# Optimization experiments

Hardware: AMD Instinct MI355X
Metric: run time of the kernel (lower is better)

The kernel has to match this reference:

```python
import jax, jax.numpy as jnp
import numpy as np

N_NODES = 100000
N_EDGES = 1600000
D_FEAT = 64
NUM_LAYERS = 3


def setup_inputs() -> dict:
    key = jax.random.key(0)
    k1, k2, k3, k4 = jax.random.split(key, 4)
    X = jax.random.normal(k1, (N_NODES, D_FEAT), dtype=jnp.float32)
    src = jax.random.randint(k2, (N_EDGES,), 0, N_NODES, dtype=jnp.int32)
    dst = jax.random.randint(k3, (N_EDGES,), 0, N_NODES, dtype=jnp.int32)
    ew = jax.random.uniform(k4, (N_EDGES,), dtype=jnp.float32)
    return {"X": X, "src": src, "dst": dst, "ew": ew}


def _spmm(X, src, dst, ew):
    # gather source features, scale by edge weight, scatter-sum into dst
    msgs = X[src] * ew[:, None]  # [E, d]
    return jax.ops.segment_sum(msgs, dst, num_segments=N_NODES)


def reference(X, src, dst, ew):
    # LightGCNConv with stack_layers=True: average of layer-0..num_layers embeddings
    X_list = [X]
    h = X
    for _ in range(NUM_LAYERS):
        h = _spmm(h, src, dst, ew)
        X_list.append(h)
    return jnp.mean(jnp.stack(X_list, axis=1), axis=1)  # [N, d]
```

## Files before the change

kernel.cpp:

```cpp
#include <hip/hip_runtime.h>
#include <hip/hip_fp16.h>

#define N_NODES 100000
#define D_FEAT  64
#define N_EDGES 1600000
#define NPB     128
#define NBUCK   ((N_NODES + NPB - 1) / NPB)
#define CAP     3072
#define CVT_BLOCKS  256
#define CVT_THREADS 1024
#define CHUNK   (N_EDGES / CVT_BLOCKS)
#define PULL_BLOCKS 2048
#define WCAP    64
#define SORT_CAP CAP

__global__ void init_bcur(int* __restrict__ bcur) {
    int t = threadIdx.x;
    if (t < NBUCK) bcur[t] = 0;
}

__global__ __launch_bounds__(CVT_THREADS) void cvt_part(const float* __restrict__ X,
                                                        __half* __restrict__ Xh,
                                                        const int* __restrict__ src,
                                                        const int* __restrict__ dst,
                                                        const float* __restrict__ ew,
                                                        int* __restrict__ bcur,
                                                        int2* __restrict__ bedges) {
    __shared__ int h[NBUCK];
    const int t = threadIdx.x;
    for (int i = t; i < NBUCK; i += CVT_THREADS) h[i] = 0;

    const int n4 = N_NODES * D_FEAT / 4;
    for (int i = blockIdx.x * CVT_THREADS + t; i < n4; i += CVT_BLOCKS * CVT_THREADS) {
        float4 v = ((const float4*)X)[i];
        ((__half2*)Xh)[2 * i]     = __floats2half2_rn(v.x, v.y);
        ((__half2*)Xh)[2 * i + 1] = __floats2half2_rn(v.z, v.w);
    }
    __syncthreads();

    const int beg = blockIdx.x * CHUNK, end = beg + CHUNK;
    for (int i = beg + t; i < end; i += CVT_THREADS)
        atomicAdd(&h[dst[i] >> 7], 1);
    __syncthreads();

    for (int i = t; i < NBUCK; i += CVT_THREADS) {
        int c = h[i];
        h[i] = c ? atomicAdd(&bcur[i], c) : 0;
    }
    __syncthreads();

    for (int i = beg + t; i < end; i += CVT_THREADS) {
        int d = dst[i];
        int b = d >> 7;
        int p = atomicAdd(&h[b], 1);
        if (p < CAP) {
            int2 e;
            e.x = src[i] | ((d & (NPB - 1)) << 17);
            e.y = __float_as_int(ew[i]);
            bedges[(size_t)b * CAP + p] = e;
        }
    }
}

__global__ void scan_bcnt(const int* __restrict__ bcnt, int* __restrict__ bptr,
                          int* __restrict__ row_ptr) {
    __shared__ int tmp[1024];
    const int t = threadIdx.x;
    int v = (t < NBUCK) ? bcnt[t] : 0;
    if (v > CAP) v = CAP;
    tmp[t] = v;
    __syncthreads();
    for (int off = 1; off < 1024; off <<= 1) {
        int u = (t >= off) ? tmp[t - off] : 0;
        __syncthreads();
        tmp[t] += u;
        __syncthreads();
    }
    if (t < NBUCK) bptr[t] = tmp[t] - v;
    if (t == NBUCK - 1) {
        bptr[NBUCK] = tmp[t];
        row_ptr[N_NODES] = tmp[t];
    }
}

__global__ __launch_bounds__(256) void sort_bucket(const int2* __restrict__ bedges,
                                                   const int* __restrict__ bcnt,
                                                   const int* __restrict__ bptr,
                                                   int2* __restrict__ sedges,
                                                   int* __restrict__ row_ptr) {
    __shared__ int cnt[NPB], sc[NPB], cur[NPB];
    __shared__ int2 buf[SORT_CAP];
    const int b = blockIdx.x, t = threadIdx.x;
    const int ibeg = b * CAP;
    const int obeg = bptr[b];
    int n = bcnt[b];
    if (n > CAP) n = CAP;

    if (t < NPB) cnt[t] = 0;
    __syncthreads();
    for (int i = t; i < n; i += 256) {
        int2 e = bedges[ibeg + i];
        buf[i] = e;
        atomicAdd(&cnt[e.x >> 17], 1);
    }
    __syncthreads();

    if (t < NPB) sc[t] = cnt[t];
    __syncthreads();
    for (int off = 1; off < NPB; off <<= 1) {
        int v = (t >= off && t < NPB) ? sc[t - off] : 0;
        __syncthreads();
        if (t < NPB) sc[t] += v;
        __syncthreads();
    }
    if (t < NPB) {
        cur[t] = sc[t] - cnt[t];
        int node = b * NPB + t;
        if (node < N_NODES) row_ptr[node] = obeg + sc[t] - cnt[t];
    }
    __syncthreads();

    for (int i = t; i < n; i += 256) {
        int2 e = buf[i];
        int p = atomicAdd(&cur[e.x >> 17], 1);
        sedges[obeg + p] = make_int2(e.x & 0x1FFFF, e.y);
    }
}

template <int MODE>
__global__ __launch_bounds__(256) void spmm_pull(const __half* __restrict__ hprev,
                                                 const int* __restrict__ row_ptr,
                                                 const int2* __restrict__ edges,
                                                 __half* __restrict__ hout,
                                                 float* __restrict__ out,
                                                 const float* __restrict__ X,
                                                 const __half* __restrict__ h1,
                                                 const __half* __restrict__ h2) {
    __shared__ int2 ebuf[4][WCAP];
    const int t    = threadIdx.x;
    const int wid  = t >> 6;
    const int lane = t & 63;
    const int half = lane >> 5;
    const int sub  = lane & 31;
    const int gw     = blockIdx.x * 4 + wid;
    const int nwaves = gridDim.x * 4;

    for (int node = gw; node < N_NODES; node += nwaves) {
        int2 bp = *(const int2*)&row_ptr[node];
        const int beg = bp.x, end = bp.y;
        const int d = end - beg;

        if (d <= WCAP) {
            const int dp = (d + 15) & ~15;
            if (lane < dp) {
                int2 e = (lane < d) ? edges[beg + lane] : make_int2(0, 0);
                ebuf[wid][lane] = e;
            }
            float ax = 0.0f, ay = 0.0f;
            const int nb = dp >> 4;
            for (int bi = 0; bi < nb; ++bi) {
                const int base = bi * 16 + half;
                unsigned tv[8]; float w[8];
                #pragma unroll
                for (int k = 0; k < 8; ++k) {
                    int2 e = ebuf[wid][base + 2 * k];
                    w[k]  = __int_as_float(e.y);
                    tv[k] = *(const unsigned*)(hprev + (((size_t)e.x << 6) | (2 * sub)));
                }
                #pragma unroll
                for (int k = 0; k < 8; ++k) {
                    float2 f = __half22float2(*(__half2*)&tv[k]);
                    ax += f.x * w[k];
                    ay += f.y * w[k];
                }
            }
            ax += __shfl_xor(ax, 32);
            ay += __shfl_xor(ay, 32);
            if (half == 0) {
                size_t bo = (size_t)node * 32 + sub;
                if (MODE == 2) {
                    float2 x  = ((const float2*)X)[bo];
                    float2 f1 = __half22float2(((const __half2*)h1)[bo]);
                    float2 f2 = __half22float2(((const __half2*)h2)[bo]);
                    ((float2*)out)[bo] = make_float2((x.x + f1.x + f2.x + ax) * 0.25f,
                                                     (x.y + f1.y + f2.y + ay) * 0.25f);
                } else {
                    ((__half2*)hout)[bo] = __floats2half2_rn(ax, ay);
                }
            }
        } else {
            float ax = 0.0f, ay = 0.0f;
            for (int j = beg; j < end; j += 16) {
                unsigned tv[8]; float w[8];
                #pragma unroll
                for (int k = 0; k < 8; ++k) {
                    int i0 = j + 2 * k, i1 = i0 + 1;
                    int2 e0 = edges[(i0 < end) ? i0 : beg];
                    int2 e1 = edges[(i1 < end) ? i1 : beg];
                    int s = half ? e1.x : e0.x;
                    float w0 = (i0 < end) ? __int_as_float(e0.y) : 0.0f;
                    float w1 = (i1 < end) ? __int_as_float(e1.y) : 0.0f;
                    w[k] = half ? w1 : w0;
                    tv[k] = *(const unsigned*)(hprev + (((size_t)s << 6) | (2 * sub)));
                }
                #pragma unroll
                for (int k = 0; k < 8; ++k) {
                    float2 f = __half22float2(*(__half2*)&tv[k]);
                    ax += f.x * w[k];
                    ay += f.y * w[k];
                }
            }
            ax += __shfl_xor(ax, 32);
            ay += __shfl_xor(ay, 32);
            if (half == 0) {
                size_t bo = (size_t)node * 32 + sub;
                if (MODE == 2) {
                    float2 x  = ((const float2*)X)[bo];
                    float2 f1 = __half22float2(((const __half2*)h1)[bo]);
                    float2 f2 = __half22float2(((const __half2*)h2)[bo]);
                    ((float2*)out)[bo] = make_float2((x.x + f1.x + f2.x + ax) * 0.25f,
                                                     (x.y + f1.y + f2.y + ay) * 0.25f);
                } else {
                    ((__half2*)hout)[bo] = __floats2half2_rn(ax, ay);
                }
            }
        }
    }
}

extern "C" void kernel_launch(void* const* d_in, const int* in_sizes, int n_in,
                              void* d_out, int out_size, void* d_ws, size_t ws_size,
                              hipStream_t stream) {
    const float* X   = (const float*)d_in[0];
    const int*   src = (const int*)  d_in[1];
    const int*   dst = (const int*)  d_in[2];
    const float* ew  = (const float*)d_in[3];
    float* out = (float*)d_out;

    const size_t feat = (size_t)N_NODES * D_FEAT;

    char* p = (char*)d_ws;
    __half* hA     = (__half*)p; p += feat * sizeof(__half);
    __half* hB     = (__half*)p; p += feat * sizeof(__half);
    __half* Xh     = (__half*)p; p += feat * sizeof(__half);
    int2*  sedges  = (int2*)p;   p += (size_t)N_EDGES * sizeof(int2);
    int*   row_ptr = (int*)p;    p += ((size_t)N_NODES + 1) * 4;
    int*   bcur    = (int*)p;    p += (size_t)NBUCK * 4;
    int*   bptr    = (int*)p;    p += ((size_t)NBUCK + 1) * 4;

    int2* bedges = (int2*)hA;

    init_bcur <<<1, 1024, 0, stream>>>(bcur);
    cvt_part  <<<CVT_BLOCKS, CVT_THREADS, 0, stream>>>(X, Xh, src, dst, ew, bcur, bedges);
    scan_bcnt <<<1, 1024, 0, stream>>>(bcur, bptr, row_ptr);
    sort_bucket<<<NBUCK, 256, 0, stream>>>(bedges, bcur, bptr, sedges, row_ptr);

    spmm_pull<0><<<PULL_BLOCKS, 256, 0, stream>>>(Xh, row_ptr, sedges, hA, out, X, hA, hB);
    spmm_pull<1><<<PULL_BLOCKS, 256, 0, stream>>>(hA, row_ptr, sedges, hB, out, X, hA, hB);
    spmm_pull<2><<<PULL_BLOCKS, 256, 0, stream>>>(hB, row_ptr, sedges, (__half*)nullptr, out, X, hA, hB);
}
```

Baseline: 229.6 us.

## Drop bucket scan kernel, sort buckets in place, use per-node (offset,count) pointers

Removes the single-block scan kernel by keeping edges in fixed-capacity per-bucket slots and sorting each bucket in place, with per-node (start, degree) pairs replacing the compacted row_ptr. The partition kernel now uses 500 blocks with each thread handling exactly four edges via vectorized int4 loads. This saves a kernel launch and a serial scan, and avoids a separate compacted edge buffer. In exchange the edge array is sparse (padded to CAP per bucket), which the SpMM loop reads only through the node pointers.

```diff
diff --git a/kernel.cpp b/kernel.cpp
--- a/kernel.cpp
+++ b/kernel.cpp
@@ -7,12 +7,11 @@
 #define NPB     128
 #define NBUCK   ((N_NODES + NPB - 1) / NPB)
 #define CAP     3072
-#define CVT_BLOCKS  256
+#define CVT_BLOCKS  500
 #define CVT_THREADS 1024
 #define CHUNK   (N_EDGES / CVT_BLOCKS)
 #define PULL_BLOCKS 2048
 #define WCAP    64
-#define SORT_CAP CAP
 
 __global__ void init_bcur(int* __restrict__ bcur) {
     int t = threadIdx.x;
@@ -25,7 +24,7 @@
                                                         const int* __restrict__ dst,
                                                         const float* __restrict__ ew,
                                                         int* __restrict__ bcur,
-                                                        int2* __restrict__ bedges) {
+                                                        int2* __restrict__ edges_p) {
     __shared__ int h[NBUCK];
     const int t = threadIdx.x;
     for (int i = t; i < NBUCK; i += CVT_THREADS) h[i] = 0;
@@ -38,68 +37,55 @@
     }
     __syncthreads();
 
-    const int beg = blockIdx.x * CHUNK, end = beg + CHUNK;
-    for (int i = beg + t; i < end; i += CVT_THREADS)
-        atomicAdd(&h[dst[i] >> 7], 1);
-    __syncthreads();
-
-    for (int i = t; i < NBUCK; i += CVT_THREADS) {
-        int c = h[i];
-        h[i] = c ? atomicAdd(&bcur[i], c) : 0;
-    }
-    __syncthreads();
-
-    for (int i = beg + t; i < end; i += CVT_THREADS) {
-        int d = dst[i];
-        int b = d >> 7;
-        int p = atomicAdd(&h[b], 1);
-        if (p < CAP) {
-            int2 e;
-            e.x = src[i] | ((d & (NPB - 1)) << 17);
-            e.y = __float_as_int(ew[i]);
-            bedges[(size_t)b * CAP + p] = e;
-        }
-    }
-}
-
-__global__ void scan_bcnt(const int* __restrict__ bcnt, int* __restrict__ bptr,
-                          int* __restrict__ row_ptr) {
-    __shared__ int tmp[1024];
-    const int t = threadIdx.x;
-    int v = (t < NBUCK) ? bcnt[t] : 0;
-    if (v > CAP) v = CAP;
-    tmp[t] = v;
-    __syncthreads();
-    for (int off = 1; off < 1024; off <<= 1) {
-        int u = (t >= off) ? tmp[t - off] : 0;
-        __syncthreads();
-        tmp[t] += u;
-        __syncthreads();
-    }
-    if (t < NBUCK) bptr[t] = tmp[t] - v;
-    if (t == NBUCK - 1) {
-        bptr[NBUCK] = tmp[t];
-        row_ptr[N_NODES] = tmp[t];
-    }
-}
-
-__global__ __launch_bounds__(256) void sort_bucket(const int2* __restrict__ bedges,
-                                                   const int* __restrict__ bcnt,
-                                                   const int* __restrict__ bptr,
-                                                   int2* __restrict__ sedges,
-                                                   int* __restrict__ row_ptr) {
+    const int beg = blockIdx.x * CHUNK;
+    const int base = beg + 4 * t;
+    const bool act = (4 * t < CHUNK);
+
+    int4 d4;
+    if (act) {
+        d4 = *(const int4*)(dst + base);
+        atomicAdd(&h[d4.x >> 7], 1);
+        atomicAdd(&h[d4.y >> 7], 1);
+        atomicAdd(&h[d4.z >> 7], 1);
+        atomicAdd(&h[d4.w >> 7], 1);
+    }
+    __syncthreads();
+
+    if (t < NBUCK) {
+        int c = h[t];
+        h[t] = c ? atomicAdd(&bcur[t], c) : 0;
+    }
+    __syncthreads();
+
+    if (act) {
+        int4   s4 = *(const int4*)(src + base);
+        float4 w4 = *(const float4*)(ew + base);
+        int b, p;
+        b = d4.x >> 7; p = atomicAdd(&h[b], 1);
+        if (p < CAP) edges_p[(size_t)b * CAP + p] = make_int2(s4.x | ((d4.x & 127) << 17), __float_as_int(w4.x));
+        b = d4.y >> 7; p = atomicAdd(&h[b], 1);
+        if (p < CAP) edges_p[(size_t)b * CAP + p] = make_int2(s4.y | ((d4.y & 127) << 17), __float_as_int(w4.y));
+        b = d4.z >> 7; p = atomicAdd(&h[b], 1);
+        if (p < CAP) edges_p[(size_t)b * CAP + p] = make_int2(s4.z | ((d4.z & 127) << 17), __float_as_int(w4.z));
+        b = d4.w >> 7; p = atomicAdd(&h[b], 1);
+        if (p < CAP) edges_p[(size_t)b * CAP + p] = make_int2(s4.w | ((d4.w & 127) << 17), __float_as_int(w4.w));
+    }
+}
+
+__global__ __launch_bounds__(256) void sort_bucket(int2* __restrict__ edges_p,
+                                                   const int* __restrict__ bcur,
+                                                   int2* __restrict__ nodeptr) {
     __shared__ int cnt[NPB], sc[NPB], cur[NPB];
-    __shared__ int2 buf[SORT_CAP];
+    __shared__ int2 buf[CAP];
     const int b = blockIdx.x, t = threadIdx.x;
-    const int ibeg = b * CAP;
-    const int obeg = bptr[b];
-    int n = bcnt[b];
+    const int beg = b * CAP;
+    int n = bcur[b];
     if (n > CAP) n = CAP;
 
     if (t < NPB) cnt[t] = 0;
     __syncthreads();
     for (int i = t; i < n; i += 256) {
-        int2 e = bedges[ibeg + i];
+        int2 e = edges_p[beg + i];
         buf[i] = e;
         atomicAdd(&cnt[e.x >> 17], 1);
     }
@@ -116,20 +102,20 @@
     if (t < NPB) {
         cur[t] = sc[t] - cnt[t];
         int node = b * NPB + t;
-        if (node < N_NODES) row_ptr[node] = obeg + sc[t] - cnt[t];
+        if (node < N_NODES) nodeptr[node] = make_int2(beg + sc[t] - cnt[t], cnt[t]);
     }
     __syncthreads();
 
     for (int i = t; i < n; i += 256) {
         int2 e = buf[i];
         int p = atomicAdd(&cur[e.x >> 17], 1);
-        sedges[obeg + p] = make_int2(e.x & 0x1FFFF, e.y);
+        edges_p[beg + p] = make_int2(e.x & 0x1FFFF, e.y);
     }
 }
 
 template <int MODE>
 __global__ __launch_bounds__(256) void spmm_pull(const __half* __restrict__ hprev,
-                                                 const int* __restrict__ row_ptr,
+                                                 const int2* __restrict__ nodeptr,
                                                  const int2* __restrict__ edges,
                                                  __half* __restrict__ hout,
                                                  float* __restrict__ out,
@@ -146,9 +132,8 @@
     const int nwaves = gridDim.x * 4;
 
     for (int node = gw; node < N_NODES; node += nwaves) {
-        int2 bp = *(const int2*)&row_ptr[node];
-        const int beg = bp.x, end = bp.y;
-        const int d = end - beg;
+        int2 np = nodeptr[node];
+        const int beg = np.x, d = np.y;
 
         if (d <= WCAP) {
             const int dp = (d + 15) & ~15;
@@ -189,6 +174,7 @@
                 }
             }
         } else {
+            const int end = beg + d;
             float ax = 0.0f, ay = 0.0f;
             for (int j = beg; j < end; j += 16) {
                 unsigned tv[8]; float w[8];
@@ -240,22 +226,18 @@
     const size_t feat = (size_t)N_NODES * D_FEAT;
 
     char* p = (char*)d_ws;
-    __half* hA     = (__half*)p; p += feat * sizeof(__half);
-    __half* hB     = (__half*)p; p += feat * sizeof(__half);
-    __half* Xh     = (__half*)p; p += feat * sizeof(__half);
-    int2*  sedges  = (int2*)p;   p += (size_t)N_EDGES * sizeof(int2);
-    int*   row_ptr = (int*)p;    p += ((size_t)N_NODES + 1) * 4;
-    int*   bcur    = (int*)p;    p += (size_t)NBUCK * 4;
-    int*   bptr    = (int*)p;    p += ((size_t)NBUCK + 1) * 4;
-
-    int2* bedges = (int2*)hA;
-
-    init_bcur <<<1, 1024, 0, stream>>>(bcur);
-    cvt_part  <<<CVT_BLOCKS, CVT_THREADS, 0, stream>>>(X, Xh, src, dst, ew, bcur, bedges);
-    scan_bcnt <<<1, 1024, 0, stream>>>(bcur, bptr, row_ptr);
-    sort_bucket<<<NBUCK, 256, 0, stream>>>(bedges, bcur, bptr, sedges, row_ptr);
-
-    spmm_pull<0><<<PULL_BLOCKS, 256, 0, stream>>>(Xh, row_ptr, sedges, hA, out, X, hA, hB);
-    spmm_pull<1><<<PULL_BLOCKS, 256, 0, stream>>>(hA, row_ptr, sedges, hB, out, X, hA, hB);
-    spmm_pull<2><<<PULL_BLOCKS, 256, 0, stream>>>(hB, row_ptr, sedges, (__half*)nullptr, out, X, hA, hB);
-}
+    __half* hA      = (__half*)p; p += feat * sizeof(__half);
+    __half* hB      = (__half*)p; p += feat * sizeof(__half);
+    __half* Xh      = (__half*)p; p += feat * sizeof(__half);
+    int2*  edges_p  = (int2*)p;   p += (size_t)NBUCK * CAP * sizeof(int2);
+    int2*  nodeptr  = (int2*)p;   p += (size_t)N_NODES * sizeof(int2);
+    int*   bcur     = (int*)p;    p += (size_t)NBUCK * 4;
+
+    init_bcur  <<<1, 1024, 0, stream>>>(bcur);
+    cvt_part   <<<CVT_BLOCKS, CVT_THREADS, 0, stream>>>(X, Xh, src, dst, ew, bcur, edges_p);
+    sort_bucket<<<NBUCK, 256, 0, stream>>>(edges_p, bcur, nodeptr);
+
+    spmm_pull<0><<<PULL_BLOCKS, 256, 0, stream>>>(Xh, nodeptr, edges_p, hA, out, X, hA, hB);
+    spmm_pull<1><<<PULL_BLOCKS, 256, 0, stream>>>(hA, nodeptr, edges_p, hB, out, X, hA, hB);
+    spmm_pull<2><<<PULL_BLOCKS, 256, 0, stream>>>(hB, nodeptr, edges_p, (__half*)nullptr, out, X, hA, hB);
+}
```

New measurement: 222.9 us. -2.9%, faster.
